# Kernel optimization log

Measured on AMD Instinct MI355X. Metric: run time of the kernel, lower is better.

## Reference

```python
import jax, jax.numpy as jnp
import numpy as np

NUM_HEADS = 16

def setup_inputs() -> dict:
    key = jax.random.key(0)
    ks = jax.random.split(key, 6)
    b, t, d = 2, 2048, 1024
    s = 0.02
    return {
        "x": jax.random.normal(ks[0], (b, t, d), jnp.float32),
        "Wq": jax.random.normal(ks[1], (d, d), jnp.float32) * s,
        "Wk": jax.random.normal(ks[2], (d, d), jnp.float32) * s,
        "Wv": jax.random.normal(ks[3], (d, d), jnp.float32) * s,
        "Wo": jax.random.normal(ks[4], (d, d), jnp.float32) * s,
        "bo": jnp.zeros((d,), jnp.float32),
    }

def reference(x, Wq, Wk, Wv, Wo, bo):
    b, t, d = x.shape
    h = NUM_HEADS
    hd = d // h  # head_dim = d_out / num_heads
    # torch nn.Linear: y = x @ W.T (qkv_bias=False)
    def split_heads(y):
        return y.reshape(b, t, h, hd).transpose(0, 2, 1, 3)  # [b,h,t,hd]
    q = split_heads(x @ Wq.T)
    k = split_heads(x @ Wk.T)
    v = split_heads(x @ Wv.T)
    scale = 1.0 / jnp.sqrt(jnp.asarray(hd, x.dtype))
    # NOTE: original forward computes but never applies the causal mask or dropout
    scores = jnp.einsum('bhqd,bhkd->bhqk', q, k) * scale
    attn = jax.nn.softmax(scores, axis=-1)
    ctx = jnp.einsum('bhqk,bhkd->bhqd', attn, v)
    ctx = ctx.transpose(0, 2, 1, 3).reshape(b, t, d)
    return ctx @ Wo.T + bo
```

## Files before the change

### kernel.cpp

```cpp
#include <hip/hip_runtime.h>
#include <hip/hip_bf16.h>
#include <math.h>
#include <stdint.h>
#include <string.h>

#define TSEQ 2048
#define DMODEL 1024
#define NH 16
#define HD 64
#define BROWS 4096
#define BH 32

typedef __attribute__((ext_vector_type(8))) short short8;
typedef __attribute__((ext_vector_type(4))) float floatx4;

#define MFMA16 __builtin_amdgcn_mfma_f32_16x16x32_bf16
#define SWZ8(r, q) ((((q) ^ ((r) & 7)) * 8))

#define QSCALE 0.18033688011112042f

__device__ __forceinline__ unsigned short bf16_rne(float f) {
    uint32_t u = __float_as_uint(f);
    u += 0x7FFFu + ((u >> 16) & 1u);
    return (unsigned short)(u >> 16);
}

__device__ __forceinline__ uint32_t pack_bf16x2(float a, float b) {
    __hip_bfloat162 h = __float22bfloat162_rn(float2{a, b});
    uint32_t r;
    memcpy(&r, &h, 4);
    return r;
}

__device__ __forceinline__ void split_bf16(float f, short& hi, short& lo) {
    uint32_t u = __float_as_uint(f);
    hi = (short)(u >> 16);
    float hif = __uint_as_float(u & 0xFFFF0000u);
    lo = (short)bf16_rne(f - hif);
}

__device__ __forceinline__ void async16(const void* g, void* l) {
    __builtin_amdgcn_global_load_lds(
        (__attribute__((address_space(1))) const uint32_t*)g,
        (__attribute__((address_space(3))) uint32_t*)l, 16, 0, 0);
}

struct PackArgs {
    const float4* x;
    ushort4* xb;
    const float4* w[3];
    ushort4* wb[3];
    const float4* wo;
    ushort4* woh;
    ushort4* wol;
};
__global__ __launch_bounds__(256) void pack_all(PackArgs a) {
    const int y = blockIdx.y;
    const int base = blockIdx.x * 256 + threadIdx.x;
    if (y == 0) {
#pragma unroll
        for (int it = 0; it < 4; ++it) {
            int i = base + it * 262144;
            float4 f = a.x[i];
            a.xb[i] = make_ushort4(bf16_rne(f.x), bf16_rne(f.y),
                                   bf16_rne(f.z), bf16_rne(f.w));
        }
    } else if (y <= 3) {
        int w = y - 1;
        float4 f = a.w[w][base];
        a.wb[w][base] = make_ushort4(bf16_rne(f.x), bf16_rne(f.y),
                                     bf16_rne(f.z), bf16_rne(f.w));
    } else {
        float4 f = a.wo[base];
        short h0, l0, h1, l1, h2, l2, h3, l3;
        split_bf16(f.x, h0, l0); split_bf16(f.y, h1, l1);
        split_bf16(f.z, h2, l2); split_bf16(f.w, h3, l3);
        a.woh[base] = make_ushort4(h0, h1, h2, h3);
        a.wol[base] = make_ushort4(l0, l1, l2, l3);
    }
}

#define QSTAGE(DB, K0)                                                          \
    {                                                                           \
        _Pragma("unroll")                                                       \
        for (int j = 0; j < 4; ++j) {                                           \
            int idx = wave * 4 + j;                                             \
            int sub = idx & 15;                                                 \
            const short* s = (idx < 16) ? Asrc : Bsrc;                          \
            short* d = (idx < 16) ? sA[DB] : sB[DB];                            \
            async16(s + (size_t)(sub * 8 + srow) * K + (K0) + soff, d + sub * 512); \
        }                                                                       \
    }

__global__ __launch_bounds__(512, 4) void gemm_qkv(
    const short* __restrict__ Xb,
    const short* __restrict__ Bq, const short* __restrict__ Bk,
    const short* __restrict__ Bv,
    short* __restrict__ Qo, short* __restrict__ Ko, short* __restrict__ Vo) {
    __shared__ short sA[2][128 * 64];
    __shared__ short sB[2][128 * 64];
    const int K = DMODEL;

    const int tid = threadIdx.x;
    const int lane = tid & 63, wave = tid >> 6;
    const int quad = lane >> 4, col = lane & 15;

    const int lin = blockIdx.y * 24 + blockIdx.x;
    const int xcd = lin & 7, j8 = lin >> 3;
    const int bxp = 3 * xcd + (j8 % 3);
    const int byp = j8 / 3;
    const int m0 = byp * 128, n0 = bxp * 128;
    const int which = n0 >> 10;
    const int nn0 = n0 & 1023;
    const int wm = wave >> 1, wn = wave & 1;

    const short* B = (which == 0) ? Bq : (which == 1) ? Bk : Bv;
    const short* Asrc = Xb + (size_t)m0 * K;
    const short* Bsrc = B + (size_t)nn0 * K;

    const int srow = lane >> 3;
    const int soff = (((lane & 7) ^ srow) * 8);

    floatx4 acc[2][4] = {};

    QSTAGE(0, 0);
    for (int t = 0; t < 16; ++t) {
        const int db = t & 1;
        if (t < 15) {
            QSTAGE(db ^ 1, (t + 1) * 64);
            asm volatile("s_waitcnt vmcnt(4)" ::: "memory");
        } else {
            asm volatile("s_waitcnt vmcnt(0)" ::: "memory");
        }
        __builtin_amdgcn_s_barrier();

#pragma unroll
        for (int s2 = 0; s2 < 2; ++s2) {
            short8 a_b[2], b_b[4];
#pragma unroll
            for (int mi = 0; mi < 2; ++mi) {
                int r = wm * 32 + mi * 16 + col;
                a_b[mi] = *(const short8*)&sA[db][r * 64 + SWZ8(r, s2 * 4 + quad)];
            }
#pragma unroll
            for (int ni = 0; ni < 4; ++ni) {
                int r = wn * 64 + ni * 16 + col;
                b_b[ni] = *(const short8*)&sB[db][r * 64 + SWZ8(r, s2 * 4 + quad)];
            }
            __builtin_amdgcn_s_setprio(1);
            if (which == 2) {
#pragma unroll
                for (int mi = 0; mi < 2; ++mi)
#pragma unroll
                    for (int ni = 0; ni < 4; ++ni)
                        acc[mi][ni] = MFMA16(a_b[mi], b_b[ni], acc[mi][ni], 0, 0, 0);
            } else {
#pragma unroll
                for (int mi = 0; mi < 2; ++mi)
#pragma unroll
                    for (int ni = 0; ni < 4; ++ni)
                        acc[mi][ni] = MFMA16(b_b[ni], a_b[mi], acc[mi][ni], 0, 0, 0);
            }
            __builtin_amdgcn_s_setprio(0);
        }
        __builtin_amdgcn_s_barrier();
    }

    const int mb = m0 + wm * 32;
    const int nlb = nn0 + wn * 64;
    if (which == 2) {
#pragma unroll
        for (int ni = 0; ni < 4; ++ni) {
            int n = nlb + ni * 16 + col;
            int h = n >> 6, hd = n & 63;
#pragma unroll
            for (int mi = 0; mi < 2; ++mi) {
                int m4 = mb + mi * 16 + quad * 4;
                int b = m4 >> 11, t0 = m4 & 2047;
                int sw = (t0 & 32) | ((t0 & 12) << 1) | ((t0 & 16) >> 2);
                int tsw = (t0 & ~63) | ((((sw >> 3) ^ (hd & 7)) << 3) | (sw & 7));
                size_t row = ((size_t)(b * NH + h) * HD + hd) * TSEQ;
                *(ushort4*)&Vo[row + tsw] =
                    make_ushort4(bf16_rne(acc[mi][ni][0]), bf16_rne(acc[mi][ni][1]),
                                 bf16_rne(acc[mi][ni][2]), bf16_rne(acc[mi][ni][3]));
            }
        }
    } else {
        short* O = (which == 0) ? Qo : Ko;
        const float sc = (which == 0) ? QSCALE : 1.0f;
#pragma unroll
        for (int mi = 0; mi < 2; ++mi) {
            int m = mb + mi * 16 + col;
            int b = m >> 11, t = m & 2047;
#pragma unroll
            for (int ni = 0; ni < 4; ++ni) {
                int n = nlb + ni * 16 + quad * 4;
                int h = n >> 6, hd = n & 63;
                int hds = (which == 1) ? ((((hd >> 3) ^ (t & 7)) << 3) | (hd & 7)) : hd;
                size_t idx = ((size_t)(b * NH + h) * TSEQ + t) * HD + hds;
                *(ushort4*)&O[idx] =
                    make_ushort4(bf16_rne(acc[mi][ni][0] * sc), bf16_rne(acc[mi][ni][1] * sc),
                                 bf16_rne(acc[mi][ni][2] * sc), bf16_rne(acc[mi][ni][3] * sc));
            }
        }
    }
}

#define QK_U(DB, U, S)                                                          \
    {                                                                           \
        __builtin_amdgcn_s_setprio(1);                                          \
        _Pragma("unroll")                                                       \
        for (int k4 = 0; k4 < 4; ++k4) {                                        \
            short8 kf0 = *(const short8*)(kb0 + (DB) * 8192 + (U) * 4096 + k4 * 1024); \
            short8 kf1 = *(const short8*)(kb1 + (DB) * 8192 + (U) * 4096 + k4 * 1024); \
            S[k4] = MFMA16(kf0, qf[0], S[k4], 0, 0, 0);                         \
            S[k4] = MFMA16(kf1, qf[1], S[k4], 0, 0, 0);                         \
        }                                                                       \
        __builtin_amdgcn_s_setprio(0);                                          \
    }

#define EXPPACK_C(S, C, PFW)                                                    \
    {                                                                           \
        float p0 = __builtin_amdgcn_exp2f(S[2 * (C)][0]);                       \
        float p1 = __builtin_amdgcn_exp2f(S[2 * (C)][1]);                       \
        float p2 = __builtin_amdgcn_exp2f(S[2 * (C)][2]);                       \
        float p3 = __builtin_amdgcn_exp2f(S[2 * (C)][3]);                       \
        float p4 = __builtin_amdgcn_exp2f(S[2 * (C) + 1][0]);                   \
        float p5 = __builtin_amdgcn_exp2f(S[2 * (C) + 1][1]);                   \
        float p6 = __builtin_amdgcn_exp2f(S[2 * (C) + 1][2]);                   \
        float p7 = __builtin_amdgcn_exp2f(S[2 * (C) + 1][3]);                   \
        PFW.w[0] = pack_bf16x2(p0, p1);                                         \
        PFW.w[1] = pack_bf16x2(p2, p3);                                         \
        PFW.w[2] = pack_bf16x2(p4, p5);                                         \
        PFW.w[3] = pack_bf16x2(p6, p7);                                         \
    }

#define PV_C(DB, U, C, PFW)                                                     \
    {                                                                           \
        const short* vbc = (C) ? vb1 : vb0;                                     \
        __builtin_amdgcn_s_setprio(1);                                          \
        lacc = MFMA16(ones.v, PFW.v, lacc, 0, 0, 0);                            \
        _Pragma("unroll")                                                       \
        for (int ni = 0; ni < 4; ++ni) {                                        \
            short8 vf = *(const short8*)(vbc + (DB) * 8192 + (U) * 4096 + ni * 1024); \
            O[ni] = MFMA16(vf, PFW.v, O[ni], 0, 0, 0);                          \
        }                                                                       \
        __builtin_amdgcn_s_setprio(0);                                          \
    }

typedef union { short8 v; uint32_t w[4]; } pfu;

#define ATTN_COMPUTE(DB)                                                        \
    {                                                                           \
        floatx4 sa[4] = {};                                                     \
        QK_U(DB, 0, sa);                                                        \
        pfu pfA0, pfA1;                                                         \
        EXPPACK_C(sa, 0, pfA0);                                                 \
        EXPPACK_C(sa, 1, pfA1);                                                 \
        floatx4 sb[4] = {};                                                     \
        QK_U(DB, 1, sb);                                                        \
              \
        pfu pfB0, pfB1;                                                         \
        PV_C(DB, 0, 0, pfA0);                                                   \
        EXPPACK_C(sb, 0, pfB0);                                                 \
        PV_C(DB, 0, 1, pfA1);                                                   \
        EXPPACK_C(sb, 1, pfB1);                                                 \
        PV_C(DB, 1, 0, pfB0);                                                   \
        PV_C(DB, 1, 1, pfB1);                                                   \
    }

#define ASTAGE(LB)                                                              \
    {                                                                           \
        async16(g0, (LB) + 0 * 512);                                            \
        async16(g1, (LB) + 1 * 512);                                            \
        async16(g2, (LB) + 2 * 512);                                            \
        async16(g3, (LB) + 3 * 512);                                            \
        g0 += ktstep; g1 += ktstep; g2 += ktstep; g3 += ktstep;                 \
    }

__global__ __launch_bounds__(512, 4) void attn_bf16(
    const short* __restrict__ Qb, const short* __restrict__ Kb,
    const short* __restrict__ Vb, short* __restrict__ Cb) {
    __shared__ short sK[2][2][64 * 64];
    __shared__ short sV[2][2][64 * 64];

    const int tid = threadIdx.x;
    const int lane = tid & 63, wave = tid >> 6;
    const int quad = lane >> 4, col = lane & 15;
    const int qt = blockIdx.x, bh = blockIdx.y;
    const size_t bhoff = (size_t)bh * TSEQ * HD;

    const size_t qrow = (size_t)(qt * 128 + wave * 16 + col) * HD;
    short8 qf[2];
#pragma unroll
    for (int c = 0; c < 2; ++c)
        qf[c] = *(const short8*)&Qb[bhoff + qrow + c * 32 + quad * 8];

    const int srow = lane >> 3;
    const int schunk = (lane & 7) * 8;

    const int isV = wave >> 2;
    const int tl = (wave >> 1) & 1;
    const int sb = (wave & 1) * 4;

    const short *g0, *g1, *g2, *g3;
    size_t ktstep;
    if (!isV) {
        g0 = Kb + bhoff + (size_t)(tl * 64 + (sb + 0) * 8 + srow) * HD + schunk;
        g1 = Kb + bhoff + (size_t)(tl * 64 + (sb + 1) * 8 + srow) * HD + schunk;
        g2 = Kb + bhoff + (size_t)(tl * 64 + (sb + 2) * 8 + srow) * HD + schunk;
        g3 = Kb + bhoff + (size_t)(tl * 64 + (sb + 3) * 8 + srow) * HD + schunk;
        ktstep = (size_t)128 * HD;
    } else {
        g0 = Vb + bhoff + (size_t)((sb + 0) * 8 + srow) * TSEQ + tl * 64 + schunk;
        g1 = Vb + bhoff + (size_t)((sb + 1) * 8 + srow) * TSEQ + tl * 64 + schunk;
        g2 = Vb + bhoff + (size_t)((sb + 2) * 8 + srow) * TSEQ + tl * 64 + schunk;
        g3 = Vb + bhoff + (size_t)((sb + 3) * 8 + srow) * TSEQ + tl * 64 + schunk;
        ktstep = 128;
    }
    short* lb0_ = isV ? &sV[0][tl][sb * 512] : &sK[0][tl][sb * 512];
    short* lb1_ = isV ? &sV[1][tl][sb * 512] : &sK[1][tl][sb * 512];

    const int ch0 = ((quad ^ (col & 7)) << 3);
    const int ch1 = (((4 + quad) ^ (col & 7)) << 3);
    const short* kb0 = &sK[0][0][col * 64 + ch0];
    const short* kb1 = &sK[0][0][col * 64 + ch1];
    const short* vb0 = &sV[0][0][col * 64 + ch0];
    const short* vb1 = &sV[0][0][col * 64 + ch1];

    union { short8 v; short s[8]; } ones;
#pragma unroll
    for (int j = 0; j < 8; ++j) ones.s[j] = (short)0x3F80;

    floatx4 lacc = {};
    floatx4 O[4] = {};

    ASTAGE(lb0_);

    for (int kt2 = 0; kt2 < 8; ++kt2) {
        ASTAGE(lb1_);
        asm volatile("s_waitcnt vmcnt(4)" ::: "memory");
        __builtin_amdgcn_s_barrier();
        ATTN_COMPUTE(0);
        __builtin_amdgcn_s_barrier();

        if (kt2 < 7) {
            ASTAGE(lb0_);
            asm volatile("s_waitcnt vmcnt(4)" ::: "memory");
        } else {
            asm volatile("s_waitcnt vmcnt(0)" ::: "memory");
        }
        __builtin_amdgcn_s_barrier();
        ATTN_COMPUTE(1);
        __builtin_amdgcn_s_barrier();
    }

    const float inv = 1.0f / lacc[0];

    const int b = bh >> 4, h = bh & 15;
    const int trow = qt * 128 + wave * 16 + col;
    const size_t obase = (size_t)(b * TSEQ + trow) * DMODEL + h * 64;
#pragma unroll
    for (int ni = 0; ni < 4; ++ni) {
        uint2 pk;
        pk.x = pack_bf16x2(O[ni][0] * inv, O[ni][1] * inv);
        pk.y = pack_bf16x2(O[ni][2] * inv, O[ni][3] * inv);
        *(uint2*)&Cb[obase + ni * 16 + quad * 4] = pk;
    }
}

#define OSTAGE(DB, K0)                                                          \
    {                                                                           \
        _Pragma("unroll")                                                       \
        for (int j = 0; j < 8; ++j) {                                           \
            int idx = wave * 8 + j;                                             \
            int buf = (idx < 16) ? 0 : (idx < 24) ? 1 : 2;                      \
            int sub = (buf == 0) ? idx : (buf == 1) ? idx - 16 : idx - 24;      \
            const short* s = (buf == 0) ? Asrc : (buf == 1) ? Bhsrc : Blsrc;    \
            short* d = (buf == 0) ? sA[DB] : (buf == 1) ? sBh[DB] : sBl[DB];    \
            async16(s + (size_t)(sub * 8 + srow) * K + (K0) + soff, d + sub * 512); \
        }                                                                       \
    }

__global__ __launch_bounds__(256) void gemm_out(
    const short* __restrict__ Ab,
    const short* __restrict__ Bh, const short* __restrict__ Bl,
    const float* __restrict__ bias, float* __restrict__ Of) {
    __shared__ short sA[2][128 * 64];
    __shared__ short sBh[2][64 * 64];
    __shared__ short sBl[2][64 * 64];
    const int K = DMODEL, N = DMODEL;

    const int tid = threadIdx.x;
    const int lane = tid & 63, wave = tid >> 6;
    const int quad = lane >> 4, col = lane & 15;

    const int lin = blockIdx.y * 16 + blockIdx.x;
    const int xcd = lin & 7, j8 = lin >> 3;
    const int bxp = 2 * xcd + (j8 & 1);
    const int byp = j8 >> 1;
    const int m0 = byp * 128, n0 = bxp * 64;
    const int wm = wave >> 1, wn = wave & 1;

    const short* Asrc = Ab + (size_t)m0 * K;
    const short* Bhsrc = Bh + (size_t)n0 * K;
    const short* Blsrc = Bl + (size_t)n0 * K;
    const int srow = lane >> 3;
    const int soff = (((lane & 7) ^ srow) * 8);

    floatx4 acc[4][2] = {};

    OSTAGE(0, 0);
    for (int t = 0; t < 16; ++t) {
        const int db = t & 1;
        if (t < 15) {
            OSTAGE(db ^ 1, (t + 1) * 64);
            asm volatile("s_waitcnt vmcnt(8)" ::: "memory");
        } else {
            asm volatile("s_waitcnt vmcnt(0)" ::: "memory");
        }
        __builtin_amdgcn_s_barrier();

#pragma unroll
        for (int s2 = 0; s2 < 2; ++s2) {
            short8 a_b[4], b_h[2], b_l[2];
#pragma unroll
            for (int mi = 0; mi < 4; ++mi) {
                int r = wm * 64 + mi * 16 + col;
                a_b[mi] = *(const short8*)&sA[db][r * 64 + SWZ8(r, s2 * 4 + quad)];
            }
#pragma unroll
            for (int ni = 0; ni < 2; ++ni) {
                int r = wn * 32 + ni * 16 + col;
                b_h[ni] = *(const short8*)&sBh[db][r * 64 + SWZ8(r, s2 * 4 + quad)];
                b_l[ni] = *(const short8*)&sBl[db][r * 64 + SWZ8(r, s2 * 4 + quad)];
            }
            __builtin_amdgcn_s_setprio(1);
#pragma unroll
            for (int mi = 0; mi < 4; ++mi)
#pragma unroll
                for (int ni = 0; ni < 2; ++ni) {
                    acc[mi][ni] = MFMA16(b_h[ni], a_b[mi], acc[mi][ni], 0, 0, 0);
                    acc[mi][ni] = MFMA16(b_l[ni], a_b[mi], acc[mi][ni], 0, 0, 0);
                }
            __builtin_amdgcn_s_setprio(0);
        }
        __builtin_amdgcn_s_barrier();
    }

    const int mb = m0 + wm * 64, nb = n0 + wn * 32;
#pragma unroll
    for (int mi = 0; mi < 4; ++mi) {
        int m = mb + mi * 16 + col;
#pragma unroll
        for (int ni = 0; ni < 2; ++ni) {
            int n = nb + ni * 16 + quad * 4;
            float4 bv = *(const float4*)&bias[n];
            float4 o = make_float4(acc[mi][ni][0] + bv.x, acc[mi][ni][1] + bv.y,
                                   acc[mi][ni][2] + bv.z, acc[mi][ni][3] + bv.w);
            *(float4*)&Of[(size_t)m * N + n] = o;
        }
    }
}

extern "C" void kernel_launch(void* const* d_in, const int* in_sizes, int n_in,
                              void* d_out, int out_size, void* d_ws, size_t ws_size,
                              hipStream_t stream) {
    const float* x  = (const float*)d_in[0];
    const float* Wq = (const float*)d_in[1];
    const float* Wk = (const float*)d_in[2];
    const float* Wv = (const float*)d_in[3];
    const float* Wo = (const float*)d_in[4];
    const float* bo = (const float*)d_in[5];
    float* out = (float*)d_out;

    const size_t NX = (size_t)BROWS * DMODEL;
    const size_t NW = (size_t)DMODEL * DMODEL;
    short* p = (short*)d_ws;
    short *xb = p;
    short *wqb = xb + NX;
    short *wkb = wqb + NW;
    short *wvb = wkb + NW;
    short *woh = wvb + NW; short *wol = woh + NW;
    short *qb = wol + NW;
    short *kb = qb + NX;
    short *vb = kb + NX;
    short *cb = vb + NX;

    PackArgs pa;
    pa.x = (const float4*)x; pa.xb = (ushort4*)xb;
    pa.w[0] = (const float4*)Wq; pa.wb[0] = (ushort4*)wqb;
    pa.w[1] = (const float4*)Wk; pa.wb[1] = (ushort4*)wkb;
    pa.w[2] = (const float4*)Wv; pa.wb[2] = (ushort4*)wvb;
    pa.wo = (const float4*)Wo; pa.woh = (ushort4*)woh; pa.wol = (ushort4*)wol;
    pack_all<<<dim3(1024, 5), dim3(256), 0, stream>>>(pa);

    gemm_qkv<<<dim3(3 * DMODEL / 128, BROWS / 128), dim3(512), 0, stream>>>(
        xb, wqb, wkb, wvb, qb, kb, vb);

    attn_bf16<<<dim3(TSEQ / 128, BH), dim3(512), 0, stream>>>(qb, kb, vb, cb);

    gemm_out<<<dim3(DMODEL / 64, BROWS / 128), dim3(256), 0, stream>>>(cb, woh, wol, bo, out);
}
```

Baseline: 180.4 us.

## Halve wave count in QKV GEMM and attention, doubling per-wave tile work

```diff
diff --git a/kernel.cpp b/kernel.cpp
--- a/kernel.cpp
+++ b/kernel.cpp
@@ -83,8 +83,8 @@
 #define QSTAGE(DB, K0)                                                          \
     {                                                                           \
         _Pragma("unroll")                                                       \
-        for (int j = 0; j < 4; ++j) {                                           \
-            int idx = wave * 4 + j;                                             \
+        for (int j = 0; j < 8; ++j) {                                           \
+            int idx = wave * 8 + j;                                             \
             int sub = idx & 15;                                                 \
             const short* s = (idx < 16) ? Asrc : Bsrc;                          \
             short* d = (idx < 16) ? sA[DB] : sB[DB];                            \
@@ -92,7 +92,7 @@
         }                                                                       \
     }
 
-__global__ __launch_bounds__(512, 4) void gemm_qkv(
+__global__ __launch_bounds__(256) void gemm_qkv(
     const short* __restrict__ Xb,
     const short* __restrict__ Bq, const short* __restrict__ Bk,
     const short* __restrict__ Bv,
@@ -121,14 +121,14 @@
     const int srow = lane >> 3;
     const int soff = (((lane & 7) ^ srow) * 8);
 
-    floatx4 acc[2][4] = {};
+    floatx4 acc[4][4] = {};
 
     QSTAGE(0, 0);
     for (int t = 0; t < 16; ++t) {
         const int db = t & 1;
         if (t < 15) {
             QSTAGE(db ^ 1, (t + 1) * 64);
-            asm volatile("s_waitcnt vmcnt(4)" ::: "memory");
+            asm volatile("s_waitcnt vmcnt(8)" ::: "memory");
         } else {
             asm volatile("s_waitcnt vmcnt(0)" ::: "memory");
         }
@@ -136,10 +136,10 @@
 
 #pragma unroll
         for (int s2 = 0; s2 < 2; ++s2) {
-            short8 a_b[2], b_b[4];
-#pragma unroll
-            for (int mi = 0; mi < 2; ++mi) {
-                int r = wm * 32 + mi * 16 + col;
+            short8 a_b[4], b_b[4];
+#pragma unroll
+            for (int mi = 0; mi < 4; ++mi) {
+                int r = wm * 64 + mi * 16 + col;
                 a_b[mi] = *(const short8*)&sA[db][r * 64 + SWZ8(r, s2 * 4 + quad)];
             }
 #pragma unroll
@@ -150,13 +150,13 @@
             __builtin_amdgcn_s_setprio(1);
             if (which == 2) {
 #pragma unroll
-                for (int mi = 0; mi < 2; ++mi)
+                for (int mi = 0; mi < 4; ++mi)
 #pragma unroll
                     for (int ni = 0; ni < 4; ++ni)
                         acc[mi][ni] = MFMA16(a_b[mi], b_b[ni], acc[mi][ni], 0, 0, 0);
             } else {
 #pragma unroll
-                for (int mi = 0; mi < 2; ++mi)
+                for (int mi = 0; mi < 4; ++mi)
 #pragma unroll
                     for (int ni = 0; ni < 4; ++ni)
                         acc[mi][ni] = MFMA16(b_b[ni], a_b[mi], acc[mi][ni], 0, 0, 0);
@@ -166,7 +166,7 @@
         __builtin_amdgcn_s_barrier();
     }
 
-    const int mb = m0 + wm * 32;
+    const int mb = m0 + wm * 64;
     const int nlb = nn0 + wn * 64;
     if (which == 2) {
 #pragma unroll
@@ -174,7 +174,7 @@
             int n = nlb + ni * 16 + col;
             int h = n >> 6, hd = n & 63;
 #pragma unroll
-            for (int mi = 0; mi < 2; ++mi) {
+            for (int mi = 0; mi < 4; ++mi) {
                 int m4 = mb + mi * 16 + quad * 4;
                 int b = m4 >> 11, t0 = m4 & 2047;
                 int sw = (t0 & 32) | ((t0 & 12) << 1) | ((t0 & 16) >> 2);
@@ -189,7 +189,7 @@
         short* O = (which == 0) ? Qo : Ko;
         const float sc = (which == 0) ? QSCALE : 1.0f;
 #pragma unroll
-        for (int mi = 0; mi < 2; ++mi) {
+        for (int mi = 0; mi < 4; ++mi) {
             int m = mb + mi * 16 + col;
             int b = m >> 11, t = m & 2047;
 #pragma unroll
@@ -206,15 +206,17 @@
     }
 }
 
-#define QK_U(DB, U, S)                                                          \
+#define QK2_U(DB, U, SA, SB)                                                    \
     {                                                                           \
         __builtin_amdgcn_s_setprio(1);                                          \
         _Pragma("unroll")                                                       \
         for (int k4 = 0; k4 < 4; ++k4) {                                        \
             short8 kf0 = *(const short8*)(kb0 + (DB) * 8192 + (U) * 4096 + k4 * 1024); \
             short8 kf1 = *(const short8*)(kb1 + (DB) * 8192 + (U) * 4096 + k4 * 1024); \
-            S[k4] = MFMA16(kf0, qf[0], S[k4], 0, 0, 0);                         \
-            S[k4] = MFMA16(kf1, qf[1], S[k4], 0, 0, 0);                         \
+            SA[k4] = MFMA16(kf0, qfA[0], SA[k4], 0, 0, 0);                      \
+            SA[k4] = MFMA16(kf1, qfA[1], SA[k4], 0, 0, 0);                      \
+            SB[k4] = MFMA16(kf0, qfB[0], SB[k4], 0, 0, 0);                      \
+            SB[k4] = MFMA16(kf1, qfB[1], SB[k4], 0, 0, 0);                      \
         }                                                                       \
         __builtin_amdgcn_s_setprio(0);                                          \
     }
@@ -235,15 +237,17 @@
         PFW.w[3] = pack_bf16x2(p6, p7);                                         \
     }
 
-#define PV_C(DB, U, C, PFW)                                                     \
+#define PV2_C(DB, U, C, FA, FB)                                                 \
     {                                                                           \
         const short* vbc = (C) ? vb1 : vb0;                                     \
         __builtin_amdgcn_s_setprio(1);                                          \
-        lacc = MFMA16(ones.v, PFW.v, lacc, 0, 0, 0);                            \
+        laccA = MFMA16(ones.v, FA.v, laccA, 0, 0, 0);                           \
+        laccB = MFMA16(ones.v, FB.v, laccB, 0, 0, 0);                           \
         _Pragma("unroll")                                                       \
         for (int ni = 0; ni < 4; ++ni) {                                        \
             short8 vf = *(const short8*)(vbc + (DB) * 8192 + (U) * 4096 + ni * 1024); \
-            O[ni] = MFMA16(vf, PFW.v, O[ni], 0, 0, 0);                          \
+            OA[ni] = MFMA16(vf, FA.v, OA[ni], 0, 0, 0);                         \
+            OB[ni] = MFMA16(vf, FB.v, OB[ni], 0, 0, 0);                         \
         }                                                                       \
         __builtin_amdgcn_s_setprio(0);                                          \
     }
@@ -252,33 +256,36 @@
 
 #define ATTN_COMPUTE(DB)                                                        \
     {                                                                           \
-        floatx4 sa[4] = {};                                                     \
-        QK_U(DB, 0, sa);                                                        \
-        pfu pfA0, pfA1;                                                         \
-        EXPPACK_C(sa, 0, pfA0);                                                 \
-        EXPPACK_C(sa, 1, pfA1);                                                 \
-        floatx4 sb[4] = {};                                                     \
-        QK_U(DB, 1, sb);                                                        \
+        floatx4 saA[4] = {}, saB[4] = {};                                       \
+        QK2_U(DB, 0, saA, saB);                                                 \
+        pfu fA0, fA1, fB0, fB1;                                                 \
+        EXPPACK_C(saA, 0, fA0);                                                 \
+        EXPPACK_C(saA, 1, fA1);                                                 \
+        EXPPACK_C(saB, 0, fB0);                                                 \
+        EXPPACK_C(saB, 1, fB1);                                                 \
+        floatx4 sbA[4] = {}, sbB[4] = {};                                       \
+        QK2_U(DB, 1, sbA, sbB);                                                 \
               \
-        pfu pfB0, pfB1;                                                         \
-        PV_C(DB, 0, 0, pfA0);                                                   \
-        EXPPACK_C(sb, 0, pfB0);                                                 \
-        PV_C(DB, 0, 1, pfA1);                                                   \
-        EXPPACK_C(sb, 1, pfB1);                                                 \
-        PV_C(DB, 1, 0, pfB0);                                                   \
-        PV_C(DB, 1, 1, pfB1);                                                   \
+        pfu gA0, gA1, gB0, gB1;                                                 \
+        PV2_C(DB, 0, 0, fA0, fB0);                                              \
+        EXPPACK_C(sbA, 0, gA0);                                                 \
+        EXPPACK_C(sbB, 0, gB0);                                                 \
+        PV2_C(DB, 0, 1, fA1, fB1);                                              \
+        EXPPACK_C(sbA, 1, gA1);                                                 \
+        EXPPACK_C(sbB, 1, gB1);                                                 \
+        PV2_C(DB, 1, 0, gA0, gB0);                                              \
+        PV2_C(DB, 1, 1, gA1, gB1);                                              \
     }
 
 #define ASTAGE(LB)                                                              \
     {                                                                           \
-        async16(g0, (LB) + 0 * 512);                                            \
-        async16(g1, (LB) + 1 * 512);                                            \
-        async16(g2, (LB) + 2 * 512);                                            \
-        async16(g3, (LB) + 3 * 512);                                            \
-        g0 += ktstep; g1 += ktstep; g2 += ktstep; g3 += ktstep;                 \
-    }
-
-__global__ __launch_bounds__(512, 4) void attn_bf16(
+        _Pragma("unroll")                                                       \
+        for (int j = 0; j < 8; ++j)                                             \
+            async16(gb + (size_t)j * gj, (LB) + j * 512);                       \
+        gb += ktstep;                                                           \
+    }
+
+__global__ __launch_bounds__(256, 2) void attn_bf16(
     const short* __restrict__ Qb, const short* __restrict__ Kb,
     const short* __restrict__ Vb, short* __restrict__ Cb) {
     __shared__ short sK[2][2][64 * 64];
@@ -290,36 +297,32 @@
     const int qt = blockIdx.x, bh = blockIdx.y;
     const size_t bhoff = (size_t)bh * TSEQ * HD;
 
-    const size_t qrow = (size_t)(qt * 128 + wave * 16 + col) * HD;
-    short8 qf[2];
-#pragma unroll
-    for (int c = 0; c < 2; ++c)
-        qf[c] = *(const short8*)&Qb[bhoff + qrow + c * 32 + quad * 8];
+    const size_t qrowA = (size_t)(qt * 128 + wave * 32 + col) * HD;
+    const size_t qrowB = qrowA + (size_t)16 * HD;
+    short8 qfA[2], qfB[2];
+#pragma unroll
+    for (int c = 0; c < 2; ++c) {
+        qfA[c] = *(const short8*)&Qb[bhoff + qrowA + c * 32 + quad * 8];
+        qfB[c] = *(const short8*)&Qb[bhoff + qrowB + c * 32 + quad * 8];
+    }
 
     const int srow = lane >> 3;
     const int schunk = (lane & 7) * 8;
 
-    const int isV = wave >> 2;
-    const int tl = (wave >> 1) & 1;
-    const int sb = (wave & 1) * 4;
-
-    const short *g0, *g1, *g2, *g3;
-    size_t ktstep;
+    const int isV = wave >> 1, tl = wave & 1;
+    const short* gb;
+    size_t gj, ktstep;
     if (!isV) {
-        g0 = Kb + bhoff + (size_t)(tl * 64 + (sb + 0) * 8 + srow) * HD + schunk;
-        g1 = Kb + bhoff + (size_t)(tl * 64 + (sb + 1) * 8 + srow) * HD + schunk;
-        g2 = Kb + bhoff + (size_t)(tl * 64 + (sb + 2) * 8 + srow) * HD + schunk;
-        g3 = Kb + bhoff + (size_t)(tl * 64 + (sb + 3) * 8 + srow) * HD + schunk;
+        gb = Kb + bhoff + (size_t)(tl * 64 + srow) * HD + schunk;
+        gj = (size_t)8 * HD;
         ktstep = (size_t)128 * HD;
     } else {
-        g0 = Vb + bhoff + (size_t)((sb + 0) * 8 + srow) * TSEQ + tl * 64 + schunk;
-        g1 = Vb + bhoff + (size_t)((sb + 1) * 8 + srow) * TSEQ + tl * 64 + schunk;
-        g2 = Vb + bhoff + (size_t)((sb + 2) * 8 + srow) * TSEQ + tl * 64 + schunk;
-        g3 = Vb + bhoff + (size_t)((sb + 3) * 8 + srow) * TSEQ + tl * 64 + schunk;
+        gb = Vb + bhoff + (size_t)srow * TSEQ + tl * 64 + schunk;
+        gj = (size_t)8 * TSEQ;
         ktstep = 128;
     }
-    short* lb0_ = isV ? &sV[0][tl][sb * 512] : &sK[0][tl][sb * 512];
-    short* lb1_ = isV ? &sV[1][tl][sb * 512] : &sK[1][tl][sb * 512];
+    short* lb0_ = isV ? sV[0][tl] : sK[0][tl];
+    short* lb1_ = isV ? sV[1][tl] : sK[1][tl];
 
     const int ch0 = ((quad ^ (col & 7)) << 3);
     const int ch1 = (((4 + quad) ^ (col & 7)) << 3);
@@ -332,21 +335,21 @@
 #pragma unroll
     for (int j = 0; j < 8; ++j) ones.s[j] = (short)0x3F80;
 
-    floatx4 lacc = {};
-    floatx4 O[4] = {};
+    floatx4 laccA = {}, laccB = {};
+    floatx4 OA[4] = {}, OB[4] = {};
 
     ASTAGE(lb0_);
 
     for (int kt2 = 0; kt2 < 8; ++kt2) {
         ASTAGE(lb1_);
-        asm volatile("s_waitcnt vmcnt(4)" ::: "memory");
+        asm volatile("s_waitcnt vmcnt(8)" ::: "memory");
         __builtin_amdgcn_s_barrier();
         ATTN_COMPUTE(0);
         __builtin_amdgcn_s_barrier();
 
         if (kt2 < 7) {
             ASTAGE(lb0_);
-            asm volatile("s_waitcnt vmcnt(4)" ::: "memory");
+            asm volatile("s_waitcnt vmcnt(8)" ::: "memory");
         } else {
             asm volatile("s_waitcnt vmcnt(0)" ::: "memory");
         }
@@ -355,17 +358,23 @@
         __builtin_amdgcn_s_barrier();
     }
 
-    const float inv = 1.0f / lacc[0];
+    const float invA = 1.0f / laccA[0];
+    const float invB = 1.0f / laccB[0];
 
     const int b = bh >> 4, h = bh & 15;
-    const int trow = qt * 128 + wave * 16 + col;
-    const size_t obase = (size_t)(b * TSEQ + trow) * DMODEL + h * 64;
+    const int trowA = qt * 128 + wave * 32 + col;
+    const size_t obaseA = (size_t)(b * TSEQ + trowA) * DMODEL + h * 64;
+    const size_t obaseB = obaseA + (size_t)16 * DMODEL;
 #pragma unroll
     for (int ni = 0; ni < 4; ++ni) {
         uint2 pk;
-        pk.x = pack_bf16x2(O[ni][0] * inv, O[ni][1] * inv);
-        pk.y = pack_bf16x2(O[ni][2] * inv, O[ni][3] * inv);
-        *(uint2*)&Cb[obase + ni * 16 + quad * 4] = pk;
+        pk.x = pack_bf16x2(OA[ni][0] * invA, OA[ni][1] * invA);
+        pk.y = pack_bf16x2(OA[ni][2] * invA, OA[ni][3] * invA);
+        *(uint2*)&Cb[obaseA + ni * 16 + quad * 4] = pk;
+        uint2 pk2;
+        pk2.x = pack_bf16x2(OB[ni][0] * invB, OB[ni][1] * invB);
+        pk2.y = pack_bf16x2(OB[ni][2] * invB, OB[ni][3] * invB);
+        *(uint2*)&Cb[obaseB + ni * 16 + quad * 4] = pk2;
     }
 }
 
@@ -495,10 +504,10 @@
     pa.wo = (const float4*)Wo; pa.woh = (ushort4*)woh; pa.wol = (ushort4*)wol;
     pack_all<<<dim3(1024, 5), dim3(256), 0, stream>>>(pa);
 
-    gemm_qkv<<<dim3(3 * DMODEL / 128, BROWS / 128), dim3(512), 0, stream>>>(
+    gemm_qkv<<<dim3(3 * DMODEL / 128, BROWS / 128), dim3(256), 0, stream>>>(
         xb, wqb, wkb, wvb, qb, kb, vb);
 
-    attn_bf16<<<dim3(TSEQ / 128, BH), dim3(512), 0, stream>>>(qb, kb, vb, cb);
+    attn_bf16<<<dim3(TSEQ / 128, BH), dim3(256), 0, stream>>>(qb, kb, vb, cb);
 
     gemm_out<<<dim3(DMODEL / 64, BROWS / 128), dim3(256), 0, stream>>>(cb, woh, wol, bo, out);
 }
```

Result: no change. 178.6 us (-1.0%).
